# Kernel tuning notes

Hardware: AMD Instinct MI355X
Metric: run time of the kernel (lower is better)

The kernel has to match this reference:

```python
import jax, jax.numpy as jnp
import numpy as np

NUM_HEADS = 4
LN_EPS = 1e-5


def setup_inputs() -> dict:
    key = jax.random.key(0)
    ks = jax.random.split(key, 12)
    B, S, D = 8, 2048, 256
    Dh = D // NUM_HEADS
    s = 0.02
    return {
        "descriptors": jax.random.normal(ks[0], (B, S, D), jnp.float32),
        # cached rotary embedding (cos, sin) pair broadcastable over heads
        "keypoints": jax.random.normal(ks[1], (2, B, 1, S, Dh), jnp.float32),
        "Wqkv_w": jax.random.normal(ks[2], (3 * D, D), jnp.float32) * s,
        "Wqkv_b": jax.random.normal(ks[3], (3 * D,), jnp.float32) * s,
        "Wo_w": jax.random.normal(ks[4], (D, D), jnp.float32) * s,
        "Wo_b": jax.random.normal(ks[5], (D,), jnp.float32) * s,
        "W1_w": jax.random.normal(ks[6], (2 * D, 2 * D), jnp.float32) * s,
        "W1_b": jax.random.normal(ks[7], (2 * D,), jnp.float32) * s,
        "ln_g": jnp.ones((2 * D,), jnp.float32),
        "ln_b": jnp.zeros((2 * D,), jnp.float32),
        "W2_w": jax.random.normal(ks[8], (D, 2 * D), jnp.float32) * s,
        "W2_b": jax.random.normal(ks[9], (D,), jnp.float32) * s,
    }


def _rotate_half(x):
    # pairwise rotation: (x0,x1,x2,x3,...) -> (-x1,x0,-x3,x2,...)
    xr = x.reshape(x.shape[:-1] + (x.shape[-1] // 2, 2))
    return jnp.stack((-xr[..., 1], xr[..., 0]), axis=-1).reshape(x.shape)


def reference(descriptors, keypoints, Wqkv_w, Wqkv_b, Wo_w, Wo_b,
              W1_w, W1_b, ln_g, ln_b, W2_w, W2_b):
    B, S, D = descriptors.shape
    H = NUM_HEADS
    Dh = D // H
    # fused QKV projection; torch layout: last dim = (H, Dh, 3) interleaved
    qkv = descriptors @ Wqkv_w.T + Wqkv_b           # [B,S,3D]
    qkv = qkv.reshape(B, S, H, Dh, 3).transpose(0, 2, 1, 3, 4)  # [B,H,S,Dh,3]
    q, k, v = qkv[..., 0], qkv[..., 1], qkv[..., 2]
    # rotary embedding on q, k
    cos, sin = keypoints[0], keypoints[1]           # [B,1,S,Dh]
    q = q * cos + _rotate_half(q) * sin
    k = k * cos + _rotate_half(k) * sin
    # scaled dot-product attention
    scale = jnp.float32(Dh) ** -0.5
    sim = jnp.einsum('bhid,bhjd->bhij', q, k) * scale
    attn = jax.nn.softmax(sim, axis=-1)
    ctx = jnp.einsum('bhij,bhjd->bhid', attn, v)    # [B,H,S,Dh]
    ctx = ctx.transpose(0, 2, 1, 3).reshape(B, S, D)
    message = ctx @ Wo_w.T + Wo_b
    # FFN over concat(descriptors, message)
    x = jnp.concatenate([descriptors, message], axis=-1)  # [B,S,2D]
    x = x @ W1_w.T + W1_b
    mu = jnp.mean(x, axis=-1, keepdims=True)
    var = jnp.var(x, axis=-1, keepdims=True)
    x = (x - mu) * jax.lax.rsqrt(var + LN_EPS) * ln_g + ln_b
    x = jax.nn.gelu(x, approximate=False)
    x = x @ W2_w.T + W2_b
    return descriptors + x
```

## Files before the change

### kernel.cpp

```cpp
#include <hip/hip_runtime.h>
#include <math.h>

#define B_  8
#define S_  2048
#define D_  256
#define H_  4
#define DH  64
#define M_  (B_ * S_)
#define QS  4194304

typedef __attribute__((ext_vector_type(8))) short bf16x8;
typedef __attribute__((ext_vector_type(4))) float f32x4;
typedef unsigned short u16;
typedef unsigned int   u32;

#define AS1 __attribute__((address_space(1)))
#define AS3 __attribute__((address_space(3)))

__device__ __forceinline__ u16 f2bf(float x) {
    union { float f; u32 u; } c; c.f = x;
    u32 r = (c.u + 0x7fffu + ((c.u >> 16) & 1u)) >> 16;
    return (u16)r;
}
__device__ __forceinline__ float bf2f(u16 x) {
    union { u32 u; float f; } c; c.u = ((u32)x) << 16;
    return c.f;
}

__device__ __forceinline__ void gload16(const void* g, void* l) {
    __builtin_amdgcn_global_load_lds((const AS1 unsigned int*)g,
                                     (AS3 unsigned int*)l, 16, 0, 0);
}

__global__ __launch_bounds__(256) void cast5_kernel(
    const float* __restrict__ s0, u16* __restrict__ d0,
    const float* __restrict__ s1, u16* __restrict__ d1,
    const float* __restrict__ s2, u16* __restrict__ d2,
    const float* __restrict__ s3, u16* __restrict__ d3,
    const float* __restrict__ s4, u16* __restrict__ d4)
{
    int bid = blockIdx.x;
    const float* s; u16* d;
    if      (bid < 4096) { s = s0; d = d0; }
    else if (bid < 4288) { s = s1; d = d1; bid -= 4096; }
    else if (bid < 4352) { s = s2; d = d2; bid -= 4288; }
    else if (bid < 4608) { s = s3; d = d3; bid -= 4352; }
    else                 { s = s4; d = d4; bid -= 4608; }
    const int i = (bid * 256 + threadIdx.x) * 4;
    const float4 v = *(const float4*)(s + i);
    u16 o[4] = {f2bf(v.x), f2bf(v.y), f2bf(v.z), f2bf(v.w)};
    *(uint2*)(d + i) = *(const uint2*)o;
}

template <int NT, int CONCAT, int RES, int OUTBF16>
__global__ __launch_bounds__(256) void gemm_bf16(
    const u16* __restrict__ A, const u16* __restrict__ A2,
    const u16* __restrict__ W, const float* __restrict__ bias,
    const float* __restrict__ res, float* __restrict__ Cf,
    u16* __restrict__ Cb, int K, int N)
{
    __shared__ u16 As[128 * 64];
    __shared__ u16 Bs[NT * 32 * 64];
    const int tid  = threadIdx.x;
    const int w    = tid >> 6;
    const int lane = tid & 63;
    const int n    = lane & 15;
    const int quad = lane >> 4;
    const int m0   = blockIdx.x * 128;
    const int n0   = blockIdx.y * (NT * 32);
    const int m_off = (w >> 1) * 64;
    const int n_off = (w & 1) * (NT * 16);
    const int lrow = lane >> 3;
    const int lcol = (lane & 7) * 8;

    f32x4 acc[4][NT];
#pragma unroll
    for (int i = 0; i < 4; i++)
#pragma unroll
        for (int j = 0; j < NT; j++) acc[i][j] = (f32x4){0.f, 0.f, 0.f, 0.f};

    for (int k0 = 0; k0 < K; k0 += 64) {
        const u16* Asrc;
        int kb, lda;
        if (CONCAT) { Asrc = (k0 < 256) ? A : A2; kb = k0 & 255; lda = 256; }
        else        { Asrc = A; kb = k0; lda = K; }

        __syncthreads();
#pragma unroll
        for (int it = 0; it < 4; it++) {
            const int r0 = it * 32 + w * 8;
            gload16(Asrc + (size_t)(m0 + r0 + lrow) * lda + kb + lcol, &As[r0 * 64]);
        }
#pragma unroll
        for (int it = 0; it < NT; it++) {
            const int r0 = it * 32 + w * 8;
            gload16(W + (size_t)(n0 + r0 + lrow) * K + k0 + lcol, &Bs[r0 * 64]);
        }
        __syncthreads();

        bf16x8 af[4][2], bf[NT][2];
#pragma unroll
        for (int mt = 0; mt < 4; mt++)
#pragma unroll
            for (int t = 0; t < 2; t++)
                af[mt][t] = *(const bf16x8*)&As[(m_off + mt * 16 + n) * 64 + t * 32 + quad * 8];
#pragma unroll
        for (int nt = 0; nt < NT; nt++)
#pragma unroll
            for (int t = 0; t < 2; t++)
                bf[nt][t] = *(const bf16x8*)&Bs[(n_off + nt * 16 + n) * 64 + t * 32 + quad * 8];

#pragma unroll
        for (int mt = 0; mt < 4; mt++)
#pragma unroll
            for (int nt = 0; nt < NT; nt++) {
                acc[mt][nt] = __builtin_amdgcn_mfma_f32_16x16x32_bf16(af[mt][0], bf[nt][0], acc[mt][nt], 0, 0, 0);
                acc[mt][nt] = __builtin_amdgcn_mfma_f32_16x16x32_bf16(af[mt][1], bf[nt][1], acc[mt][nt], 0, 0, 0);
            }
    }

#pragma unroll
    for (int nt = 0; nt < NT; nt++) {
        const int col = n0 + n_off + nt * 16 + n;
        const float bv = bias[col];
#pragma unroll
        for (int mt = 0; mt < 4; mt++) {
#pragma unroll
            for (int r = 0; r < 4; r++) {
                const int row = m0 + m_off + mt * 16 + quad * 4 + r;
                float o = acc[mt][nt][r] + bv;
                if (RES) o += res[(size_t)row * N + col];
                if (OUTBF16) Cb[(size_t)row * N + col] = f2bf(o);
                else         Cf[(size_t)row * N + col] = o;
            }
        }
    }
}

__global__ __launch_bounds__(256) void rope_kernel(
    const u16* __restrict__ qkv, const float* __restrict__ kp,
    u16* __restrict__ q, u16* __restrict__ k, u16* __restrict__ v)
{
    const int row = blockIdx.x * 2 + (threadIdx.x >> 7);
    const int t   = threadIdx.x & 127;
    const int b   = row >> 11;
    const int s   = row & 2047;
    const int h   = t >> 5;
    const int dp  = t & 31;
    const int d   = dp * 2;

    const u16* src = qkv + (size_t)row * 768 + h * 192 + dp * 6;
    const u32 w0 = *(const u32*)(src);
    const u32 w1 = *(const u32*)(src + 2);
    const u32 w2 = *(const u32*)(src + 4);
    const float qe = bf2f((u16)w0), ke = bf2f((u16)(w0 >> 16));
    const float qo = bf2f((u16)(w1 >> 16));
    const float ko = bf2f((u16)w2);

    const size_t kidx = ((size_t)b * S_ + s) * DH + d;
    const float2 cs = *(const float2*)(kp + kidx);
    const float2 sn = *(const float2*)(kp + (size_t)B_ * S_ * DH + kidx);

    const float qe2 = (qe * cs.x - qo * sn.x) * 0.125f;
    const float qo2 = (qo * cs.y + qe * sn.y) * 0.125f;
    const float ke2 = ke * cs.x - ko * sn.x;
    const float ko2 = ko * cs.y + ke * sn.y;

    const size_t oidx = (((size_t)(b * H_ + h)) * S_ + s) * DH + d;
    *(u32*)(q + oidx) = (u32)f2bf(qe2) | ((u32)f2bf(qo2) << 16);
    *(u32*)(k + oidx) = (u32)f2bf(ke2) | ((u32)f2bf(ko2) << 16);
    *(u32*)(v + oidx) = (w1 & 0xffffu) | (w2 & 0xffff0000u);
}

__global__ __launch_bounds__(256) void vtrans_kernel(
    const u16* __restrict__ v, u16* __restrict__ vt)
{
    const int bh = blockIdx.x;
    const int s  = blockIdx.y * 256 + threadIdx.x;
    const u16* src = v + ((size_t)bh * S_ + s) * DH;
    u16* dst = vt + (size_t)bh * DH * S_ + s;
#pragma unroll
    for (int g = 0; g < 8; g++) {
        const uint4 vv = *(const uint4*)(src + g * 8);
        const u16* us = (const u16*)&vv;
#pragma unroll
        for (int i = 0; i < 8; i++) dst[(size_t)(g * 8 + i) * S_] = us[i];
    }
}

__global__ __launch_bounds__(256, 2) void attn_kernel(
    const u16* __restrict__ q, const u16* __restrict__ k,
    const u16* __restrict__ vt, u16* __restrict__ ctx)
{
    __shared__ u16 ks[128 * 64];
    __shared__ u16 qs[128 * 64];
    __shared__ u16 vs[64 * 128];
    __shared__ u16 ps[128 * 128];

    const int tid  = threadIdx.x;
    const int w    = tid >> 6;
    const int lane = tid & 63;
    const int n    = lane & 15;
    const int quad = lane >> 4;
    const int lrow = lane >> 3;
    const int vrow = lane >> 4;
    const int bh   = blockIdx.x;
    const int q0   = blockIdx.y * 128;
    const int b    = bh >> 2;
    const int h    = bh & 3;
    const int nsw  = n & 7;

    const int kcol  = (((lane & 7) ^ lrow) * 8);
    const int vcol0 = (((lane & 15) ^ vrow) * 8);
    const int vcol1 = (((lane & 15) ^ (4 + vrow)) * 8);

    const u16* qbase = q  + (size_t)bh * S_ * DH;
    const u16* kbase = k  + (size_t)bh * S_ * DH;
    const u16* vbase = vt + (size_t)bh * DH * S_;

#pragma unroll
    for (int it = 0; it < 4; it++) {
        const int idx = it * 256 + tid;
        const int row = idx >> 3;
        const int c8  = idx & 7;
        *(uint4*)&qs[row * 64 + ((c8 ^ (row & 7)) * 8)] =
            *(const uint4*)(qbase + (size_t)(q0 + row) * DH + c8 * 8);
    }
    __syncthreads();

    bf16x8 qf[2][2];
#pragma unroll
    for (int mb = 0; mb < 2; mb++) {
        qf[mb][0] = *(const bf16x8*)&qs[(w * 32 + mb * 16 + n) * 64 + ((quad       ^ nsw) * 8)];
        qf[mb][1] = *(const bf16x8*)&qs[(w * 32 + mb * 16 + n) * 64 + (((4 + quad) ^ nsw) * 8)];
    }

    f32x4 o[2][4];
#pragma unroll
    for (int mb = 0; mb < 2; mb++)
#pragma unroll
        for (int j = 0; j < 4; j++) o[mb][j] = (f32x4){0.f, 0.f, 0.f, 0.f};
    float lrun[2] = {0.f, 0.f};

    for (int kb = 0; kb < S_ / 128; kb++) {
        const int k0 = kb * 128;
        __syncthreads();
#pragma unroll
        for (int it = 0; it < 4; it++) {
            const int r0 = w * 32 + it * 8;
            gload16(kbase + (size_t)(k0 + r0 + lrow) * DH + kcol, &ks[r0 * 64]);
            const int d0 = w * 16 + it * 4;
            gload16(vbase + (size_t)(d0 + vrow) * S_ + k0 + ((it & 1) ? vcol1 : vcol0),
                    &vs[d0 * 128]);
        }
        __syncthreads();

        f32x4 sacc[2][8];
#pragma unroll
        for (int mb = 0; mb < 2; mb++)
#pragma unroll
            for (int j = 0; j < 8; j++)
                sacc[mb][j] = (f32x4){-12.f, -12.f, -12.f, -12.f};
#pragma unroll
        for (int t = 0; t < 2; t++) {
#pragma unroll
            for (int j = 0; j < 8; j++) {
                const bf16x8 kf = *(const bf16x8*)
                    &ks[(16 * j + n) * 64 + (((t * 4 + quad) ^ nsw) * 8)];
                sacc[0][j] = __builtin_amdgcn_mfma_f32_16x16x32_bf16(kf, qf[0][t], sacc[0][j], 0, 0, 0);
                sacc[1][j] = __builtin_amdgcn_mfma_f32_16x16x32_bf16(kf, qf[1][t], sacc[1][j], 0, 0, 0);
            }
        }

#pragma unroll
        for (int mb = 0; mb < 2; mb++) {
            float rs = 0.f;
            const int prow = (w * 32 + mb * 16 + n) * 128;
#pragma unroll
            for (int j = 0; j < 8; j++) {
                const float e0 = __expf(sacc[mb][j][0]);
                const float e1 = __expf(sacc[mb][j][1]);
                const float e2 = __expf(sacc[mb][j][2]);
                const float e3 = __expf(sacc[mb][j][3]);
                rs += (e0 + e1) + (e2 + e3);
                uint2 pk;
                pk.x = (u32)f2bf(e0) | ((u32)f2bf(e1) << 16);
                pk.y = (u32)f2bf(e2) | ((u32)f2bf(e3) << 16);
                const int blk = (4 * j + quad) ^ (nsw << 2);
                *(uint2*)&ps[prow + blk * 4] = pk;
            }
            lrun[mb] += rs;
        }

#pragma unroll
        for (int kt = 0; kt < 4; kt++) {
            const bf16x8 pf0 = *(const bf16x8*)
                &ps[(w * 32 +      n) * 128 + ((32 * kt + 8 * quad) ^ (nsw << 4))];
            const bf16x8 pf1 = *(const bf16x8*)
                &ps[(w * 32 + 16 + n) * 128 + ((32 * kt + 8 * quad) ^ (nsw << 4))];
#pragma unroll
            for (int nt = 0; nt < 4; nt++) {
                const bf16x8 vf = *(const bf16x8*)
                    &vs[(16 * nt + n) * 128 + (((kt * 4 + quad) ^ nsw) * 8)];
                o[0][nt] = __builtin_amdgcn_mfma_f32_16x16x32_bf16(pf0, vf, o[0][nt], 0, 0, 0);
                o[1][nt] = __builtin_amdgcn_mfma_f32_16x16x32_bf16(pf1, vf, o[1][nt], 0, 0, 0);
            }
        }
    }

#pragma unroll
    for (int mb = 0; mb < 2; mb++) {
        float s = lrun[mb];
        s += __shfl_xor(s, 16);
        s += __shfl_xor(s, 32);
        lrun[mb] = s;
    }

#pragma unroll
    for (int mb = 0; mb < 2; mb++) {
#pragma unroll
        for (int r = 0; r < 4; r++) {
            const float sv = __shfl(lrun[mb], quad * 4 + r);
            const float inv = 1.f / sv;
            const int row = q0 + w * 32 + mb * 16 + quad * 4 + r;
#pragma unroll
            for (int nt = 0; nt < 4; nt++)
                ctx[((size_t)b * S_ + row) * D_ + h * DH + 16 * nt + n] = f2bf(o[mb][nt][r] * inv);
        }
    }
}

__global__ __launch_bounds__(256) void ln_gelu_kernel(
    const float* __restrict__ x, const float* __restrict__ g,
    const float* __restrict__ bt, u16* __restrict__ y)
{
    __shared__ float ss[4], sqs[4];
    const int m = blockIdx.x;
    const float* row = x + (size_t)m * 512;
    const int t = threadIdx.x;
    const float v0 = row[t];
    const float v1 = row[t + 256];
    float s  = v0 + v1;
    float sq = v0 * v0 + v1 * v1;
#pragma unroll
    for (int off = 1; off < 64; off <<= 1) {
        s  += __shfl_xor(s, off);
        sq += __shfl_xor(sq, off);
    }
    const int w = t >> 6;
    if ((t & 63) == 0) { ss[w] = s; sqs[w] = sq; }
    __syncthreads();
    s  = ss[0] + ss[1] + ss[2] + ss[3];
    sq = sqs[0] + sqs[1] + sqs[2] + sqs[3];
    const float mu   = s * (1.f / 512.f);
    const float var  = sq * (1.f / 512.f) - mu * mu;
    const float rstd = rsqrtf(var + 1e-5f);

    const float y0 = (v0 - mu) * rstd * g[t] + bt[t];
    const float y1 = (v1 - mu) * rstd * g[t + 256] + bt[t + 256];
    y[(size_t)m * 512 + t]       = f2bf(0.5f * y0 * (1.f + erff(y0 * 0.70710678118654752f)));
    y[(size_t)m * 512 + t + 256] = f2bf(0.5f * y1 * (1.f + erff(y1 * 0.70710678118654752f)));
}

extern "C" void kernel_launch(void* const* d_in, const int* in_sizes, int n_in,
                              void* d_out, int out_size, void* d_ws, size_t ws_size,
                              hipStream_t stream)
{
    const float* desc   = (const float*)d_in[0];
    const float* kp     = (const float*)d_in[1];
    const float* Wqkv_w = (const float*)d_in[2];
    const float* Wqkv_b = (const float*)d_in[3];
    const float* Wo_w   = (const float*)d_in[4];
    const float* Wo_b   = (const float*)d_in[5];
    const float* W1_w   = (const float*)d_in[6];
    const float* W1_b   = (const float*)d_in[7];
    const float* ln_g   = (const float*)d_in[8];
    const float* ln_b   = (const float*)d_in[9];
    const float* W2_w   = (const float*)d_in[10];
    const float* W2_b   = (const float*)d_in[11];
    float* out = (float*)d_out;
    float* ws  = (float*)d_ws;

    u16*   qkvb  = (u16*)ws;
    float* x1    = ws;
    u16*   x1b   = (u16*)(ws + 2 * (size_t)QS);
    u16*   qb    = (u16*)(ws + 3 * (size_t)QS);
    u16*   kb    = (u16*)(ws + (size_t)(3.5 * QS));
    u16*   vb    = (u16*)(ws + 4 * (size_t)QS);
    u16*   ctxb  = (u16*)(ws + (size_t)(4.5 * QS));
    u16*   descb = (u16*)(ws + 5 * (size_t)QS);
    u16*   msgb  = (u16*)(ws + (size_t)(5.5 * QS));
    u16*   wpool = (u16*)(ws + 6 * (size_t)QS);
    u16*   vtb   = (u16*)(ws + (size_t)(6.5 * QS));
    u16* wqkvb = wpool;
    u16* wob   = wqkvb + 196608;
    u16* w1b   = wob   + 65536;
    u16* w2b   = w1b   + 262144;

    const dim3 blk(256);

    cast5_kernel<<<dim3(4736), blk, 0, stream>>>(
        desc, descb, Wqkv_w, wqkvb, Wo_w, wob, W1_w, w1b, W2_w, w2b);

    gemm_bf16<4, 0, 0, 1><<<dim3(M_ / 128, 768 / 128), blk, 0, stream>>>(
        descb, nullptr, wqkvb, Wqkv_b, nullptr, nullptr, qkvb, 256, 768);

    rope_kernel<<<dim3(M_ / 2), blk, 0, stream>>>(qkvb, kp, qb, kb, vb);

    vtrans_kernel<<<dim3(B_ * H_, S_ / 256), blk, 0, stream>>>(vb, vtb);

    attn_kernel<<<dim3(B_ * H_, S_ / 128), blk, 0, stream>>>(qb, kb, vtb, ctxb);

    gemm_bf16<2, 0, 0, 1><<<dim3(M_ / 128, 256 / 64), blk, 0, stream>>>(
        ctxb, nullptr, wob, Wo_b, nullptr, nullptr, msgb, 256, 256);

    gemm_bf16<4, 1, 0, 0><<<dim3(M_ / 128, 512 / 128), blk, 0, stream>>>(
        descb, msgb, w1b, W1_b, nullptr, x1, nullptr, 512, 512);

    ln_gelu_kernel<<<dim3(M_), blk, 0, stream>>>(x1, ln_g, ln_b, x1b);

    gemm_bf16<2, 0, 1, 0><<<dim3(M_ / 128, 256 / 64), blk, 0, stream>>>(
        x1b, nullptr, w2b, W2_b, desc, out, nullptr, 512, 256);
}
```

Baseline: 245.2 us.

## Fold Wo projection into W1 weights and use exp2 softmax with setprio

Precomputes W1[:,256:]·Wo and a folded bias (W1_b plus W1[:,256:]·Wo_b) on device, so the FFN GEMM consumes the attention context directly and the separate Wo GEMM launch is removed. The q scale absorbs log2(e) so the softmax uses the hardware exp2 instruction, with the initial offset adjusted to match. MFMA sections in attention get s_setprio raised. This adds a small weight-combining GEMM and a serial bias dot-product in the cast kernel, and rounds the combined weight to bf16, which slightly changes numerics.

```diff
diff --git a/kernel.cpp b/kernel.cpp
--- a/kernel.cpp
+++ b/kernel.cpp
@@ -32,21 +32,58 @@
                                      (AS3 unsigned int*)l, 16, 0, 0);
 }
 
-__global__ __launch_bounds__(256) void cast5_kernel(
-    const float* __restrict__ s0, u16* __restrict__ d0,
-    const float* __restrict__ s1, u16* __restrict__ d1,
-    const float* __restrict__ s2, u16* __restrict__ d2,
-    const float* __restrict__ s3, u16* __restrict__ d3,
-    const float* __restrict__ s4, u16* __restrict__ d4)
+__global__ __launch_bounds__(256) void cast6_kernel(
+    const float* __restrict__ desc, u16* __restrict__ descb,
+    const float* __restrict__ wqkv, u16* __restrict__ wqkvb,
+    const float* __restrict__ wo,   u16* __restrict__ wotb,
+    const float* __restrict__ w1,   u16* __restrict__ w1f, u16* __restrict__ w1br,
+    const float* __restrict__ w2,   u16* __restrict__ w2b,
+    const float* __restrict__ w1_b, const float* __restrict__ wo_b,
+    float* __restrict__ bias1f, float* __restrict__ zb)
 {
     int bid = blockIdx.x;
+    const int tid = threadIdx.x;
+
+    if (bid >= 4736) {
+        const int n = (bid - 4736) * 256 + tid;
+        float acc = w1_b[n];
+        const float* wrow = w1 + (size_t)n * 512 + 256;
+#pragma unroll 4
+        for (int j = 0; j < 256; j++) acc += wrow[j] * wo_b[j];
+        bias1f[n] = acc;
+        if (bid == 4736) zb[tid] = 0.f;
+        return;
+    }
+    if (bid >= 4608) {
+        const int i = ((bid - 4608) * 256 + tid) * 4;
+        const float4 v = *(const float4*)(w2 + i);
+        u16 o[4] = {f2bf(v.x), f2bf(v.y), f2bf(v.z), f2bf(v.w)};
+        *(uint2*)(w2b + i) = *(const uint2*)o;
+        return;
+    }
+    if (bid >= 4352) {
+        const int e = ((bid - 4352) * 256 + tid) * 4;
+        const int row = e >> 9, col = e & 511;
+        const float4 v = *(const float4*)(w1 + e);
+        u16 o[4] = {f2bf(v.x), f2bf(v.y), f2bf(v.z), f2bf(v.w)};
+        if (col < 256) *(uint2*)(w1f  + (size_t)row * 512 + col)       = *(const uint2*)o;
+        else           *(uint2*)(w1br + (size_t)row * 256 + col - 256) = *(const uint2*)o;
+        return;
+    }
+    if (bid >= 4288) {
+        const int e = ((bid - 4288) * 256 + tid) * 4;
+        const int row = e >> 8, col = e & 255;
+        const float4 v = *(const float4*)(wo + e);
+        wotb[(size_t)(col + 0) * 256 + row] = f2bf(v.x);
+        wotb[(size_t)(col + 1) * 256 + row] = f2bf(v.y);
+        wotb[(size_t)(col + 2) * 256 + row] = f2bf(v.z);
+        wotb[(size_t)(col + 3) * 256 + row] = f2bf(v.w);
+        return;
+    }
     const float* s; u16* d;
-    if      (bid < 4096) { s = s0; d = d0; }
-    else if (bid < 4288) { s = s1; d = d1; bid -= 4096; }
-    else if (bid < 4352) { s = s2; d = d2; bid -= 4288; }
-    else if (bid < 4608) { s = s3; d = d3; bid -= 4352; }
-    else                 { s = s4; d = d4; bid -= 4608; }
-    const int i = (bid * 256 + threadIdx.x) * 4;
+    if (bid < 4096) { s = desc; d = descb; }
+    else            { s = wqkv; d = wqkvb; bid -= 4096; }
+    const int i = (bid * 256 + tid) * 4;
     const float4 v = *(const float4*)(s + i);
     u16 o[4] = {f2bf(v.x), f2bf(v.y), f2bf(v.z), f2bf(v.w)};
     *(uint2*)(d + i) = *(const uint2*)o;
@@ -57,7 +94,7 @@
     const u16* __restrict__ A, const u16* __restrict__ A2,
     const u16* __restrict__ W, const float* __restrict__ bias,
     const float* __restrict__ res, float* __restrict__ Cf,
-    u16* __restrict__ Cb, int K, int N)
+    u16* __restrict__ Cb, int K, int N, int ldc)
 {
     __shared__ u16 As[128 * 64];
     __shared__ u16 Bs[NT * 32 * 64];
@@ -129,13 +166,15 @@
             for (int r = 0; r < 4; r++) {
                 const int row = m0 + m_off + mt * 16 + quad * 4 + r;
                 float o = acc[mt][nt][r] + bv;
-                if (RES) o += res[(size_t)row * N + col];
-                if (OUTBF16) Cb[(size_t)row * N + col] = f2bf(o);
-                else         Cf[(size_t)row * N + col] = o;
+                if (RES) o += res[(size_t)row * ldc + col];
+                if (OUTBF16) Cb[(size_t)row * ldc + col] = f2bf(o);
+                else         Cf[(size_t)row * ldc + col] = o;
             }
         }
     }
 }
+
+#define QSCALE 0.18033688011112042f
 
 __global__ __launch_bounds__(256) void rope_kernel(
     const u16* __restrict__ qkv, const float* __restrict__ kp,
@@ -161,8 +200,8 @@
     const float2 cs = *(const float2*)(kp + kidx);
     const float2 sn = *(const float2*)(kp + (size_t)B_ * S_ * DH + kidx);
 
-    const float qe2 = (qe * cs.x - qo * sn.x) * 0.125f;
-    const float qo2 = (qo * cs.y + qe * sn.y) * 0.125f;
+    const float qe2 = (qe * cs.x - qo * sn.x) * QSCALE;
+    const float qo2 = (qo * cs.y + qe * sn.y) * QSCALE;
     const float ke2 = ke * cs.x - ko * sn.x;
     const float ko2 = ko * cs.y + ke * sn.y;
 
@@ -187,6 +226,8 @@
         for (int i = 0; i < 8; i++) dst[(size_t)(g * 8 + i) * S_] = us[i];
     }
 }
+
+#define NEG12L2E -17.312340490667562f
 
 __global__ __launch_bounds__(256, 2) void attn_kernel(
     const u16* __restrict__ q, const u16* __restrict__ k,
@@ -260,7 +301,8 @@
         for (int mb = 0; mb < 2; mb++)
 #pragma unroll
             for (int j = 0; j < 8; j++)
-                sacc[mb][j] = (f32x4){-12.f, -12.f, -12.f, -12.f};
+                sacc[mb][j] = (f32x4){NEG12L2E, NEG12L2E, NEG12L2E, NEG12L2E};
+        __builtin_amdgcn_s_setprio(1);
 #pragma unroll
         for (int t = 0; t < 2; t++) {
 #pragma unroll
@@ -271,6 +313,7 @@
                 sacc[1][j] = __builtin_amdgcn_mfma_f32_16x16x32_bf16(kf, qf[1][t], sacc[1][j], 0, 0, 0);
             }
         }
+        __builtin_amdgcn_s_setprio(0);
 
 #pragma unroll
         for (int mb = 0; mb < 2; mb++) {
@@ -278,10 +321,10 @@
             const int prow = (w * 32 + mb * 16 + n) * 128;
 #pragma unroll
             for (int j = 0; j < 8; j++) {
-                const float e0 = __expf(sacc[mb][j][0]);
-                const float e1 = __expf(sacc[mb][j][1]);
-                const float e2 = __expf(sacc[mb][j][2]);
-                const float e3 = __expf(sacc[mb][j][3]);
+                const float e0 = __builtin_amdgcn_exp2f(sacc[mb][j][0]);
+                const float e1 = __builtin_amdgcn_exp2f(sacc[mb][j][1]);
+                const float e2 = __builtin_amdgcn_exp2f(sacc[mb][j][2]);
+                const float e3 = __builtin_amdgcn_exp2f(sacc[mb][j][3]);
                 rs += (e0 + e1) + (e2 + e3);
                 uint2 pk;
                 pk.x = (u32)f2bf(e0) | ((u32)f2bf(e1) << 16);
@@ -292,6 +335,7 @@
             lrun[mb] += rs;
         }
 
+        __builtin_amdgcn_s_setprio(1);
 #pragma unroll
         for (int kt = 0; kt < 4; kt++) {
             const bf16x8 pf0 = *(const bf16x8*)
@@ -306,6 +350,7 @@
                 o[1][nt] = __builtin_amdgcn_mfma_f32_16x16x32_bf16(pf1, vf, o[1][nt], 0, 0, 0);
             }
         }
+        __builtin_amdgcn_s_setprio(0);
     }
 
 #pragma unroll
@@ -389,21 +434,27 @@
     u16*   vb    = (u16*)(ws + 4 * (size_t)QS);
     u16*   ctxb  = (u16*)(ws + (size_t)(4.5 * QS));
     u16*   descb = (u16*)(ws + 5 * (size_t)QS);
-    u16*   msgb  = (u16*)(ws + (size_t)(5.5 * QS));
+    float* bias1f = ws + (size_t)(5.5 * QS);
+    float* zb     = bias1f + 512;
     u16*   wpool = (u16*)(ws + 6 * (size_t)QS);
     u16*   vtb   = (u16*)(ws + (size_t)(6.5 * QS));
     u16* wqkvb = wpool;
-    u16* wob   = wqkvb + 196608;
-    u16* w1b   = wob   + 65536;
-    u16* w2b   = w1b   + 262144;
+    u16* w2b   = wqkvb + 196608;
+    u16* wotb  = w2b   + 131072;
+    u16* w1br  = wotb  + 65536;
+    u16* w1f   = w1br  + 131072;
 
     const dim3 blk(256);
 
-    cast5_kernel<<<dim3(4736), blk, 0, stream>>>(
-        desc, descb, Wqkv_w, wqkvb, Wo_w, wob, W1_w, w1b, W2_w, w2b);
+    cast6_kernel<<<dim3(4738), blk, 0, stream>>>(
+        desc, descb, Wqkv_w, wqkvb, Wo_w, wotb, W1_w, w1f, w1br, W2_w, w2b,
+        W1_b, Wo_b, bias1f, zb);
+
+    gemm_bf16<4, 0, 0, 1><<<dim3(4, 2), blk, 0, stream>>>(
+        w1br, nullptr, wotb, zb, nullptr, nullptr, w1f + 256, 256, 256, 512);
 
     gemm_bf16<4, 0, 0, 1><<<dim3(M_ / 128, 768 / 128), blk, 0, stream>>>(
-        descb, nullptr, wqkvb, Wqkv_b, nullptr, nullptr, qkvb, 256, 768);
+        descb, nullptr, wqkvb, Wqkv_b, nullptr, nullptr, qkvb, 256, 768, 768);
 
     rope_kernel<<<dim3(M_ / 2), blk, 0, stream>>>(qkvb, kp, qb, kb, vb);
 
@@ -411,14 +462,11 @@
 
     attn_kernel<<<dim3(B_ * H_, S_ / 128), blk, 0, stream>>>(qb, kb, vtb, ctxb);
 
-    gemm_bf16<2, 0, 0, 1><<<dim3(M_ / 128, 256 / 64), blk, 0, stream>>>(
-        ctxb, nullptr, wob, Wo_b, nullptr, nullptr, msgb, 256, 256);
-
     gemm_bf16<4, 1, 0, 0><<<dim3(M_ / 128, 512 / 128), blk, 0, stream>>>(
-        descb, msgb, w1b, W1_b, nullptr, x1, nullptr, 512, 512);
+        descb, ctxb, w1f, bias1f, nullptr, x1, nullptr, 512, 512, 512);
 
     ln_gelu_kernel<<<dim3(M_), blk, 0, stream>>>(x1, ln_g, ln_b, x1b);
 
     gemm_bf16<2, 0, 1, 0><<<dim3(M_ / 128, 256 / 64), blk, 0, stream>>>(
-        x1b, nullptr, w2b, W2_b, desc, out, nullptr, 512, 256);
-}
+        x1b, nullptr, w2b, W2_b, desc, out, nullptr, 512, 256, 256);
+}
```

Measured after the change: 244.5 us. About the same (-0.3%).
